# Kernel optimization log

Hardware: AMD Instinct MI355X
Metric: run time of the kernel (lower is better)

## Reference

```python
import jax, jax.numpy as jnp
import numpy as np

LN_EPS = 1e-5  # torch.nn.LayerNorm default

QLEN, MLEN, BATCH, D_MODEL = 1024, 1024, 8, 1024


def _ft_matrix(qlen, klen):
    """Real part of the causal Fourier matrix (imag part never contributes:
    the input is real and the module takes .real of the product)."""
    ft_len = klen - qlen + 1
    m = jnp.arange(qlen, dtype=jnp.float32)
    k = jnp.arange(ft_len, dtype=jnp.float32)
    base = jnp.cos((2.0 * float(np.pi)) * jnp.outer(m, k) / float(ft_len))
    base = base / float(np.sqrt(ft_len))                      # [qlen, ft_len]
    mat = jnp.pad(base, ((0, 0), (klen - ft_len, 0)))          # left-pad -> [qlen, klen]
    # row i rolled left by (qlen - 1 - i), vectorized as a gather
    shift = (qlen - 1) - jnp.arange(qlen)                      # [qlen]
    cols = (jnp.arange(klen)[None, :] + shift[:, None]) % klen  # [qlen, klen]
    mat = jnp.take_along_axis(mat, cols, axis=1)
    rows = jnp.arange(qlen)[:, None]
    js = jnp.arange(klen)[None, :]
    # tril(diagonal=klen-qlen) AND triu(0)  (same_length=True)
    mask = (js <= rows + (klen - qlen)) & (js >= rows)
    return jnp.where(mask, mat, jnp.float32(0.0))


def setup_inputs() -> dict:
    key = jax.random.key(0)
    k1, k2, k3 = jax.random.split(key, 3)
    return {
        "dec_inp": jax.random.normal(k1, (QLEN, BATCH, D_MODEL), dtype=jnp.float32),
        "pos_emb": jax.random.normal(k2, (QLEN + MLEN, 1, D_MODEL), dtype=jnp.float32),
        "mems": jax.random.normal(k3, (MLEN, BATCH, D_MODEL), dtype=jnp.float32),
        "gamma": jnp.ones((D_MODEL,), dtype=jnp.float32),
        "beta": jnp.zeros((D_MODEL,), dtype=jnp.float32),
        "add_position": 1,
    }


def reference(dec_inp, pos_emb, mems, gamma, beta, add_position):
    qlen = dec_inp.shape[0]
    klen = qlen + mems.shape[0]
    cat = jnp.concatenate([mems, dec_inp], axis=0)  # [klen, b, d]
    if add_position:
        cat = cat + pos_emb  # dropout is identity in eval mode
    ft_mat = _ft_matrix(qlen, klen)                 # [qlen, klen]
    ft = jnp.einsum('ml,lbd->mbd', ft_mat, cat)     # real part of complex matmul
    x = dec_inp + ft / float(np.sqrt(klen))
    mu = jnp.mean(x, axis=-1, keepdims=True)
    var = jnp.var(x, axis=-1, keepdims=True)
    return gamma * (x - mu) * jax.lax.rsqrt(var + LN_EPS) + beta
```

## Files before the change

### kernel.cpp

```cpp
#include <hip/hip_runtime.h>
#include <hip/hip_bf16.h>

#define QLEN   1024
#define MLEN   1024
#define KLEN   2048
#define BATCH  8
#define DMODEL 1024
#define NCOLS  (BATCH * DMODEL)
#define FTLEN  1025

#define BM 128
#define BN 256
#define BK 64
#define NT 18

typedef __attribute__((ext_vector_type(4))) float f32x4;
typedef __attribute__((ext_vector_type(8))) short bf16x8;

typedef __attribute__((address_space(1))) const unsigned int as1_u32;
typedef __attribute__((address_space(3))) unsigned int as3_u32;

static __device__ __forceinline__ unsigned short f2bf(float f) {
    unsigned int u = __builtin_bit_cast(unsigned int, f);
    return (unsigned short)((u + 0x7fffu + ((u >> 16) & 1u)) >> 16);
}
static __device__ __forceinline__ float bf2f(unsigned short s) {
    return __builtin_bit_cast(float, (unsigned int)s << 16);
}
static __device__ __forceinline__ unsigned int packbf(float lo, float hi) {
    return (unsigned int)f2bf(lo) | ((unsigned int)f2bf(hi) << 16);
}

__global__ __launch_bounds__(256) void prep_transpose2(
    const float* __restrict__ dec, const float* __restrict__ pos,
    const float* __restrict__ mems, const int* __restrict__ addp,
    unsigned short* __restrict__ catT)
{
    __shared__ unsigned int T2[32 * 68];
    const int tid = threadIdx.x;
    const int lt = blockIdx.x, dt = blockIdx.y, b = blockIdx.z;
    const int l0 = lt * 64, d0 = dt * 64;
    const int add_position = addp[0];

    const int dloc  = (tid & 15) * 4;
    const int lhalf = tid >> 4;

    float4 vc[2][2];
#pragma unroll
    for (int p = 0; p < 2; ++p)
#pragma unroll
        for (int jl = 0; jl < 2; ++jl) {
            const int l = l0 + p * 32 + lhalf * 2 + jl;
            const float* src = (l < MLEN)
                ? (mems + (size_t)l * NCOLS + b * DMODEL + d0 + dloc)
                : (dec + (size_t)(l - MLEN) * NCOLS + b * DMODEL + d0 + dloc);
            vc[p][jl] = *reinterpret_cast<const float4*>(src);
        }
    if (add_position) {
#pragma unroll
        for (int p = 0; p < 2; ++p)
#pragma unroll
            for (int jl = 0; jl < 2; ++jl) {
                const int l = l0 + p * 32 + lhalf * 2 + jl;
                float4 pv = *reinterpret_cast<const float4*>(
                    pos + (size_t)l * DMODEL + d0 + dloc);
                vc[p][jl].x += pv.x; vc[p][jl].y += pv.y;
                vc[p][jl].z += pv.z; vc[p][jl].w += pv.w;
            }
    }
#pragma unroll
    for (int p = 0; p < 2; ++p) {
        const int lp = p * 16 + lhalf;
        uint4 w;
        w.x = packbf(vc[p][0].x, vc[p][1].x);
        w.y = packbf(vc[p][0].y, vc[p][1].y);
        w.z = packbf(vc[p][0].z, vc[p][1].z);
        w.w = packbf(vc[p][0].w, vc[p][1].w);
        *reinterpret_cast<uint4*>(&T2[lp * 68 + dloc]) = w;
    }
    __syncthreads();
    const int d = tid >> 2;
    const size_t n = (size_t)b * DMODEL + d0 + d;
#pragma unroll
    for (int q = 0; q < 2; ++q) {
        const int c8 = (tid & 3) + 4 * q;
        uint4 o;
        o.x = T2[(c8 * 4 + 0) * 68 + d];
        o.y = T2[(c8 * 4 + 1) * 68 + d];
        o.z = T2[(c8 * 4 + 2) * 68 + d];
        o.w = T2[(c8 * 4 + 3) * 68 + d];
        *reinterpret_cast<uint4*>(&catT[n * KLEN + l0 + c8 * 8]) = o;
    }
}

__global__ __launch_bounds__(256) void fill_w(unsigned short* __restrict__ W)
{
    const int idx = blockIdx.x * 256 + threadIdx.x;
    const int m = idx >> 9;
    const int k4 = (idx & 511) * 4;
    union { unsigned short s[4]; int2 v; } u;
    for (int j = 0; j < 4; ++j) {
        const int k = k4 + j;
        const int t = k - m;
        float w = 0.0f;
        if (t >= 0 && t < FTLEN) {
            const int r = (m * t) % FTLEN;
            const float x = (float)r * (1.0f / (float)FTLEN);
            float c;
            asm("v_cos_f32 %0, %1" : "=v"(c) : "v"(x));
            w = c * 0.03123475237772121f;
        }
        u.s[j] = f2bf(w);
    }
    *reinterpret_cast<int2*>(&W[(size_t)m * KLEN + k4]) = u.v;
}

__global__ __launch_bounds__(512) void gemm_band4(
    const unsigned short* __restrict__ W,
    const unsigned short* __restrict__ catT,
    unsigned short* __restrict__ ftout)
{
    __shared__ unsigned short Alds[3][BM * BK];
    __shared__ unsigned short Blds[3][BN * BK];

    const int tid = threadIdx.x;
    const int wave = tid >> 6, lane = tid & 63;

    const int bid = blockIdx.x;
    const int xcd = bid & 7;
    const int kk = bid >> 3;
    const int m_idx = kk >> 2;
    const int n_idx = xcd * 4 + (kk & 3);
    const int m0 = m_idx * BM, n0 = n_idx * BN;
    const int wm = wave >> 2, wn = wave & 3;

    f32x4 acc[4][4];
    for (int i = 0; i < 4; ++i)
        for (int j = 0; j < 4; ++j)
            acc[i][j] = (f32x4){0.f, 0.f, 0.f, 0.f};

    const int srow = tid >> 3;
    const int scol = (((tid & 7) ^ ((tid >> 3) & 7)) * 8);
    const int fr = lane & 15;
    const int kg = lane >> 4;
    const int rswz = (fr & 7) * 8;

#define STAGE_LOAD_A(S, T, P) do {                                              \
    const int k0_ = m0 + (T) * BK;                                              \
    const int row = (P) * 64 + srow;                                            \
    __builtin_amdgcn_global_load_lds(                                           \
        (as1_u32*)(const void*)(W + (size_t)(m0 + row) * KLEN + k0_ + scol),    \
        (as3_u32*)(void*)(&Alds[S][row * BK + scol]), 16, 0, 0);                \
} while (0)
#define STAGE_LOAD_B(S, T, P) do {                                              \
    const int k0_ = m0 + (T) * BK;                                              \
    const int row = (P) * 64 + srow;                                            \
    __builtin_amdgcn_global_load_lds(                                           \
        (as1_u32*)(const void*)(catT + (size_t)(n0 + row) * KLEN + k0_ + scol), \
        (as3_u32*)(void*)(&Blds[S][row * BK + scol]), 16, 0, 0);                \
} while (0)
#define STAGE_ALL(S, T) do {                                                    \
    STAGE_LOAD_A(S, T, 0); STAGE_LOAD_A(S, T, 1);                               \
    STAGE_LOAD_B(S, T, 0); STAGE_LOAD_B(S, T, 1);                               \
    STAGE_LOAD_B(S, T, 2); STAGE_LOAD_B(S, T, 3);                               \
} while (0)

    STAGE_ALL(0, 0);
    STAGE_ALL(1, 1);

    for (int t = 0; t < NT; ++t) {
        if (t == NT - 1)
            asm volatile("s_waitcnt vmcnt(0)" ::: "memory");
        else
            asm volatile("s_waitcnt vmcnt(6)" ::: "memory");
        __builtin_amdgcn_s_barrier();

        const unsigned short* Ab = Alds[t % 3];
        const unsigned short* Bb = Blds[t % 3];
        const int s2 = (t + 2) % 3;
        const bool pf = (t + 2 < NT);

        {
            bf16x8 a[4], b[4];
#pragma unroll
            for (int f = 0; f < 4; ++f)
                a[f] = *reinterpret_cast<const bf16x8*>(
                    Ab + (wm * 64 + f * 16 + fr) * BK + ((kg * 8) ^ rswz));
#pragma unroll
            for (int f = 0; f < 4; ++f)
                b[f] = *reinterpret_cast<const bf16x8*>(
                    Bb + (wn * 64 + f * 16 + fr) * BK + ((kg * 8) ^ rswz));
            if (pf) { STAGE_LOAD_A(s2, t + 2, 0); STAGE_LOAD_B(s2, t + 2, 0); STAGE_LOAD_B(s2, t + 2, 1); }
            __builtin_amdgcn_s_barrier();
            asm volatile("s_waitcnt lgkmcnt(0)" ::: "memory");
            __builtin_amdgcn_s_setprio(1);
#pragma unroll
            for (int fm = 0; fm < 4; ++fm)
#pragma unroll
                for (int fn = 0; fn < 4; ++fn)
                    acc[fm][fn] = __builtin_amdgcn_mfma_f32_16x16x32_bf16(
                        a[fm], b[fn], acc[fm][fn], 0, 0, 0);
            __builtin_amdgcn_s_setprio(0);
            __builtin_amdgcn_s_barrier();
        }
        {
            bf16x8 a[4], b[4];
#pragma unroll
            for (int f = 0; f < 4; ++f)
                a[f] = *reinterpret_cast<const bf16x8*>(
                    Ab + (wm * 64 + f * 16 + fr) * BK + ((32 + kg * 8) ^ rswz));
#pragma unroll
            for (int f = 0; f < 4; ++f)
                b[f] = *reinterpret_cast<const bf16x8*>(
                    Bb + (wn * 64 + f * 16 + fr) * BK + ((32 + kg * 8) ^ rswz));
            if (pf) { STAGE_LOAD_A(s2, t + 2, 1); STAGE_LOAD_B(s2, t + 2, 2); STAGE_LOAD_B(s2, t + 2, 3); }
            __builtin_amdgcn_s_barrier();
            asm volatile("s_waitcnt lgkmcnt(0)" ::: "memory");
            __builtin_amdgcn_s_setprio(1);
#pragma unroll
            for (int fm = 0; fm < 4; ++fm)
#pragma unroll
                for (int fn = 0; fn < 4; ++fn)
                    acc[fm][fn] = __builtin_amdgcn_mfma_f32_16x16x32_bf16(
                        a[fm], b[fn], acc[fm][fn], 0, 0, 0);
            __builtin_amdgcn_s_setprio(0);
        }
    }
#undef STAGE_ALL
#undef STAGE_LOAD_A
#undef STAGE_LOAD_B

    const int col16 = lane & 15, rquad = lane >> 4;
#pragma unroll
    for (int fm = 0; fm < 4; ++fm)
#pragma unroll
        for (int fn = 0; fn < 4; ++fn)
#pragma unroll
            for (int j = 0; j < 4; ++j) {
                const int m = m0 + wm * 64 + fm * 16 + rquad * 4 + j;
                const int n = n0 + wn * 64 + fn * 16 + col16;
                ftout[(size_t)m * NCOLS + n] = f2bf(acc[fm][fn][j]);
            }
}

__global__ __launch_bounds__(256) void layernorm_rows(
    const unsigned short* __restrict__ ft, const float* __restrict__ dec,
    const float* __restrict__ gamma, const float* __restrict__ beta,
    float* __restrict__ out)
{
    __shared__ float ps[4], pq[4];
    const int row = blockIdx.x;
    const int tid = threadIdx.x;
    const float inv = 0.022097086912079612f;
    const size_t base = (size_t)row * DMODEL + tid * 4;
    ushort4 u = *reinterpret_cast<const ushort4*>(ft + base);
    float4 dv = *reinterpret_cast<const float4*>(dec + base);
    float vx = dv.x + bf2f(u.x) * inv;
    float vy = dv.y + bf2f(u.y) * inv;
    float vz = dv.z + bf2f(u.z) * inv;
    float vw = dv.w + bf2f(u.w) * inv;
    float s  = vx + vy + vz + vw;
    float sq = vx * vx + vy * vy + vz * vz + vw * vw;
    for (int off = 32; off > 0; off >>= 1) {
        s  += __shfl_down(s, off);
        sq += __shfl_down(sq, off);
    }
    const int wave = tid >> 6, lane = tid & 63;
    if (lane == 0) { ps[wave] = s; pq[wave] = sq; }
    __syncthreads();
    if (tid == 0) {
        float ts = ps[0] + ps[1] + ps[2] + ps[3];
        float tq = pq[0] + pq[1] + pq[2] + pq[3];
        float mu = ts * (1.0f / DMODEL);
        float var = tq * (1.0f / DMODEL) - mu * mu;
        ps[0] = mu;
        pq[0] = rsqrtf(var + 1e-5f);
    }
    __syncthreads();
    const float mu = ps[0], rs = pq[0];
    float4 g  = *reinterpret_cast<const float4*>(gamma + tid * 4);
    float4 be = *reinterpret_cast<const float4*>(beta + tid * 4);
    float4 o;
    o.x = g.x * (vx - mu) * rs + be.x;
    o.y = g.y * (vy - mu) * rs + be.y;
    o.z = g.z * (vz - mu) * rs + be.z;
    o.w = g.w * (vw - mu) * rs + be.w;
    *reinterpret_cast<float4*>(out + base) = o;
}

extern "C" void kernel_launch(void* const* d_in, const int* in_sizes, int n_in,
                              void* d_out, int out_size, void* d_ws, size_t ws_size,
                              hipStream_t stream)
{
    const float* dec   = (const float*)d_in[0];
    const float* pos   = (const float*)d_in[1];
    const float* mems  = (const float*)d_in[2];
    const float* gamma = (const float*)d_in[3];
    const float* beta  = (const float*)d_in[4];
    const int*   addp  = (const int*)d_in[5];
    float* out = (float*)d_out;

    unsigned short* catT = (unsigned short*)d_ws;
    unsigned short* Wmat = catT + (size_t)NCOLS * KLEN;
    unsigned short* ft   = Wmat + (size_t)QLEN * KLEN;

    prep_transpose2<<<dim3(32, 16, 8), 256, 0, stream>>>(dec, pos, mems, addp, catT);
    fill_w<<<2048, 256, 0, stream>>>(Wmat);
    gemm_band4<<<256, 512, 0, stream>>>(Wmat, catT, ft);
    layernorm_rows<<<8192, 256, 0, stream>>>(ft, dec, gamma, beta, out);
}
```

Before: 64.13 us.

## Fuse W-matrix fill into prep kernel and drop intra-k-step GEMM barriers

Folds the Fourier weight generation into the prep/transpose launch as an extra z-slice of 512 blocks, each writing four chunks, which removes one kernel launch. In the GEMM main loop it also removes the barrier and lgkmcnt wait between the LDS fragment reads and the MFMAs in both half-steps, along with the trailing barrier after the first half. Fewer barriers let waves overlap the MFMAs with the prefetch loads. The risk is correctness: waits on LDS reads and cross-wave ordering against the triple-buffer overwrite now depend only on the barrier that remains and on compiler-inserted waitcnts.

```diff
diff --git a/kernel.cpp b/kernel.cpp
--- a/kernel.cpp
+++ b/kernel.cpp
@@ -31,13 +31,40 @@
     return (unsigned int)f2bf(lo) | ((unsigned int)f2bf(hi) << 16);
 }
 
-__global__ __launch_bounds__(256) void prep_transpose2(
+__global__ __launch_bounds__(256) void prep_fused(
     const float* __restrict__ dec, const float* __restrict__ pos,
     const float* __restrict__ mems, const int* __restrict__ addp,
-    unsigned short* __restrict__ catT)
+    unsigned short* __restrict__ catT, unsigned short* __restrict__ W)
 {
+    const int tid = threadIdx.x;
+    if (blockIdx.z == 8) {
+        const int bchunk = (blockIdx.y * 32 + blockIdx.x) * 4;
+#pragma unroll
+        for (int r = 0; r < 4; ++r) {
+            const int idx = (bchunk + r) * 256 + tid;
+            const int m = idx >> 9;
+            const int k4 = (idx & 511) * 4;
+            union { unsigned short s[4]; int2 v; } u;
+#pragma unroll
+            for (int j = 0; j < 4; ++j) {
+                const int k = k4 + j;
+                const int t = k - m;
+                float w = 0.0f;
+                if (t >= 0 && t < FTLEN) {
+                    const int rr = (m * t) % FTLEN;
+                    const float x = (float)rr * (1.0f / (float)FTLEN);
+                    float c;
+                    asm("v_cos_f32 %0, %1" : "=v"(c) : "v"(x));
+                    w = c * 0.03123475237772121f;
+                }
+                u.s[j] = f2bf(w);
+            }
+            *reinterpret_cast<int2*>(&W[(size_t)m * KLEN + k4]) = u.v;
+        }
+        return;
+    }
+
     __shared__ unsigned int T2[32 * 68];
-    const int tid = threadIdx.x;
     const int lt = blockIdx.x, dt = blockIdx.y, b = blockIdx.z;
     const int l0 = lt * 64, d0 = dt * 64;
     const int add_position = addp[0];
@@ -93,29 +120,7 @@
     }
 }
 
-__global__ __launch_bounds__(256) void fill_w(unsigned short* __restrict__ W)
-{
-    const int idx = blockIdx.x * 256 + threadIdx.x;
-    const int m = idx >> 9;
-    const int k4 = (idx & 511) * 4;
-    union { unsigned short s[4]; int2 v; } u;
-    for (int j = 0; j < 4; ++j) {
-        const int k = k4 + j;
-        const int t = k - m;
-        float w = 0.0f;
-        if (t >= 0 && t < FTLEN) {
-            const int r = (m * t) % FTLEN;
-            const float x = (float)r * (1.0f / (float)FTLEN);
-            float c;
-            asm("v_cos_f32 %0, %1" : "=v"(c) : "v"(x));
-            w = c * 0.03123475237772121f;
-        }
-        u.s[j] = f2bf(w);
-    }
-    *reinterpret_cast<int2*>(&W[(size_t)m * KLEN + k4]) = u.v;
-}
-
-__global__ __launch_bounds__(512) void gemm_band4(
+__global__ __launch_bounds__(512) void gemm_band9(
     const unsigned short* __restrict__ W,
     const unsigned short* __restrict__ catT,
     unsigned short* __restrict__ ftout)
@@ -191,8 +196,6 @@
                 b[f] = *reinterpret_cast<const bf16x8*>(
                     Bb + (wn * 64 + f * 16 + fr) * BK + ((kg * 8) ^ rswz));
             if (pf) { STAGE_LOAD_A(s2, t + 2, 0); STAGE_LOAD_B(s2, t + 2, 0); STAGE_LOAD_B(s2, t + 2, 1); }
-            __builtin_amdgcn_s_barrier();
-            asm volatile("s_waitcnt lgkmcnt(0)" ::: "memory");
             __builtin_amdgcn_s_setprio(1);
 #pragma unroll
             for (int fm = 0; fm < 4; ++fm)
@@ -201,7 +204,6 @@
                     acc[fm][fn] = __builtin_amdgcn_mfma_f32_16x16x32_bf16(
                         a[fm], b[fn], acc[fm][fn], 0, 0, 0);
             __builtin_amdgcn_s_setprio(0);
-            __builtin_amdgcn_s_barrier();
         }
         {
             bf16x8 a[4], b[4];
@@ -214,8 +216,6 @@
                 b[f] = *reinterpret_cast<const bf16x8*>(
                     Bb + (wn * 64 + f * 16 + fr) * BK + ((32 + kg * 8) ^ rswz));
             if (pf) { STAGE_LOAD_A(s2, t + 2, 1); STAGE_LOAD_B(s2, t + 2, 2); STAGE_LOAD_B(s2, t + 2, 3); }
-            __builtin_amdgcn_s_barrier();
-            asm volatile("s_waitcnt lgkmcnt(0)" ::: "memory");
             __builtin_amdgcn_s_setprio(1);
 #pragma unroll
             for (int fm = 0; fm < 4; ++fm)
@@ -304,8 +304,7 @@
     unsigned short* Wmat = catT + (size_t)NCOLS * KLEN;
     unsigned short* ft   = Wmat + (size_t)QLEN * KLEN;
 
-    prep_transpose2<<<dim3(32, 16, 8), 256, 0, stream>>>(dec, pos, mems, addp, catT);
-    fill_w<<<2048, 256, 0, stream>>>(Wmat);
-    gemm_band4<<<256, 512, 0, stream>>>(Wmat, catT, ft);
+    prep_fused<<<dim3(32, 16, 9), 256, 0, stream>>>(dec, pos, mems, addp, catT, Wmat);
+    gemm_band9<<<256, 512, 0, stream>>>(Wmat, catT, ft);
     layernorm_rows<<<8192, 256, 0, stream>>>(ft, dec, gamma, beta, out);
 }
```

Measured after the change: 61.30 us. -4.4%, faster.
